# Optimization experiments

Measured on AMD Instinct MI355X. Metric: run time of the kernel, lower is better.

## Reference

```python
import math
import jax, jax.numpy as jnp
import numpy as np

NUM_HEADS = 16
D_MODEL = 1024
D_HEAD = 64
D_SEQ = 2048
NUM_LAYERS = 24
BATCH = 2


def setup_inputs() -> dict:
    key = jax.random.key(0)
    ks = jax.random.split(key, 10)
    s = math.sqrt(0.02)
    residual = jax.random.normal(ks[0], (BATCH, D_SEQ, D_MODEL), dtype=jnp.float32)
    W_Q = jax.random.normal(ks[1], (NUM_HEADS, D_MODEL, D_HEAD), dtype=jnp.float32) * s
    W_K = jax.random.normal(ks[2], (NUM_HEADS, D_MODEL, D_HEAD), dtype=jnp.float32) * s
    W_V = jax.random.normal(ks[3], (NUM_HEADS, D_MODEL, D_HEAD), dtype=jnp.float32) * s
    W_O = jax.random.normal(ks[4], (NUM_HEADS * D_HEAD, D_MODEL), dtype=jnp.float32) * s
    W_O = W_O / math.sqrt(NUM_LAYERS)
    b_Q = jax.random.normal(ks[5], (NUM_HEADS, D_HEAD), dtype=jnp.float32) * s
    b_K = jax.random.normal(ks[6], (NUM_HEADS, D_HEAD), dtype=jnp.float32) * s
    b_V = jax.random.normal(ks[7], (NUM_HEADS, D_HEAD), dtype=jnp.float32) * s
    b_O = jax.random.normal(ks[8], (D_MODEL,), dtype=jnp.float32) * s
    return dict(residual=residual, W_Q=W_Q, W_K=W_K, W_V=W_V, W_O=W_O,
                b_Q=b_Q, b_K=b_K, b_V=b_V, b_O=b_O)


def reference(residual, W_Q, W_K, W_V, W_O, b_Q, b_K, b_V, b_O):
    # residual: [b, s, m]; W_{Q,K,V}: [h, m, d]; b_{Q,K,V}: [h, d]
    Q = jnp.einsum('hmd,bsm->bshd', W_Q, residual) + b_Q
    K = jnp.einsum('hmd,bsm->bshd', W_K, residual) + b_K
    V = jnp.einsum('hmd,bsm->bshd', W_V, residual) + b_V
    # full causal score matrix [b, h, s_q, s_k], masked with -inf above diagonal
    QK = jnp.einsum('bqhd,bkhd->bhqk', Q, K)
    seq = residual.shape[1]
    causal = jnp.triu(jnp.ones((seq, seq), dtype=bool), k=1)  # True above diag
    QK_masked = jnp.where(causal, -jnp.inf, QK)
    soft = jax.nn.softmax(QK_masked / math.sqrt(D_HEAD), axis=-1)
    attn = jnp.einsum('bhqk,bkhd->bqhd', soft, V)  # [b, s, h, d]
    multi_head = attn.reshape(attn.shape[0], attn.shape[1], NUM_HEADS * D_HEAD)
    return jnp.einsum('em,bqe->bqm', W_O, multi_head) + b_O
```

## Files before the change

kernel.cpp:

```cpp
#include <hip/hip_runtime.h>
#include <stdint.h>

typedef unsigned short u16;
typedef _Float16 f16;
typedef __attribute__((ext_vector_type(8))) _Float16 f16x8;
typedef __attribute__((ext_vector_type(4))) float f32x4;
typedef __attribute__((ext_vector_type(4))) unsigned short u16x4;
typedef __attribute__((ext_vector_type(8))) unsigned short u16x8;
typedef __attribute__((ext_vector_type(2))) unsigned u32x2;

#define NHEADS 16
#define DMODEL 1024
#define DHEAD 64
#define SEQ 2048
#define NBATCH 2
#define MROWS (NBATCH * SEQ)
#define NQKV 3072
#define SCQ 0.18033688011112042f

__device__ __forceinline__ u16 f2h(float x) {
  union { f16 h; u16 u; } v;
  v.h = (f16)x;
  return v.u;
}

__device__ __forceinline__ void gload_lds16(const void* g, void* l) {
  __builtin_amdgcn_global_load_lds(
      (const __attribute__((address_space(1))) void*)g,
      (__attribute__((address_space(3))) void*)l, 16, 0, 0);
}

__global__ __launch_bounds__(256) void prep_kernel(
    const float* __restrict__ X,
    const float* __restrict__ WQ, const float* __restrict__ WK,
    const float* __restrict__ WV, const float* __restrict__ WO,
    u16* __restrict__ Xh, u16* __restrict__ Wqkv, u16* __restrict__ Wo) {
  __shared__ u16 lt[64][72];
  int blk = blockIdx.x;
  if (blk < 2048) {
    int i = blk * 256 + threadIdx.x;
    const f32x4* xv = (const f32x4*)(X + (size_t)i * 8);
    f32x4 a = xv[0], b = xv[1];
    u16x8 o;
    o[0] = f2h(a[0]); o[1] = f2h(a[1]); o[2] = f2h(a[2]); o[3] = f2h(a[3]);
    o[4] = f2h(b[0]); o[5] = f2h(b[1]); o[6] = f2h(b[2]); o[7] = f2h(b[3]);
    *(u16x8*)(Xh + (size_t)i * 8) = o;
  } else if (blk < 2816) {
    int bb = blk - 2048;
    int mt = bb & 15, hh = (bb >> 4) & 15, qkv = bb >> 8;
    const float* W = (qkv == 0) ? WQ : (qkv == 1) ? WK : WV;
    int m_in = threadIdx.x >> 2, dq = threadIdx.x & 3;
    const f32x4* sp4 = (const f32x4*)(W + (size_t)hh * (DMODEL * DHEAD) +
                                      (size_t)(mt * 64 + m_in) * DHEAD + dq * 16);
#pragma unroll
    for (int v4 = 0; v4 < 4; ++v4) {
      f32x4 a = sp4[v4];
#pragma unroll
      for (int j = 0; j < 4; ++j) lt[dq * 16 + v4 * 4 + j][m_in] = f2h(a[j]);
    }
    __syncthreads();
    int d_in = threadIdx.x >> 2, mq = threadIdx.x & 3;
    size_t orow = ((size_t)(qkv * 1024 + hh * 64 + d_in)) * DMODEL + mt * 64 + mq * 16;
    u16x8 o0, o1;
#pragma unroll
    for (int j = 0; j < 8; ++j) {
      o0[j] = lt[d_in][mq * 16 + j];
      o1[j] = lt[d_in][mq * 16 + 8 + j];
    }
    *(u16x8*)(Wqkv + orow) = o0;
    *(u16x8*)(Wqkv + orow + 8) = o1;
  } else {
    int bb = blk - 2816;
    int mt = bb & 15, et = bb >> 4;
    int e_in = threadIdx.x >> 2, mq = threadIdx.x & 3;
    const f32x4* sp4 = (const f32x4*)(WO + (size_t)(et * 64 + e_in) * DMODEL + mt * 64 + mq * 16);
#pragma unroll
    for (int v4 = 0; v4 < 4; ++v4) {
      f32x4 a = sp4[v4];
#pragma unroll
      for (int j = 0; j < 4; ++j) lt[mq * 16 + v4 * 4 + j][e_in] = f2h(a[j]);
    }
    __syncthreads();
    int m_in = threadIdx.x >> 2, eq = threadIdx.x & 3;
    size_t orow = (size_t)(mt * 64 + m_in) * DMODEL + et * 64 + eq * 16;
    u16x8 o0, o1;
#pragma unroll
    for (int j = 0; j < 8; ++j) {
      o0[j] = lt[m_in][eq * 16 + j];
      o1[j] = lt[m_in][eq * 16 + 8 + j];
    }
    *(u16x8*)(Wo + orow) = o0;
    *(u16x8*)(Wo + orow + 8) = o1;
  }
}

__global__ __launch_bounds__(256, 2) void gemm_qkv(
    const u16* __restrict__ A, const u16* __restrict__ Bt,
    const float* __restrict__ bq, const float* __restrict__ bk, const float* __restrict__ bv,
    u16* __restrict__ Qo, u16* __restrict__ Ko, u16* __restrict__ Vto) {
  __shared__ u16 lds[2][8192];
  const int tid = threadIdx.x;
  const int wid = tid >> 6, lane = tid & 63, lr = lane & 15, lg = lane >> 4;
  const int wr = wid >> 1, wc = wid & 1;
  const int brow = blockIdx.y * 128, bcol = blockIdx.x * 128;

  f32x4 acc[4][4];
#pragma unroll
  for (int i = 0; i < 4; ++i)
#pragma unroll
    for (int j = 0; j < 4; ++j) acc[i][j] = (f32x4){0.f, 0.f, 0.f, 0.f};

#define STAGE(buf, kt)                                                               \
  {                                                                                  \
    _Pragma("unroll") for (int i = 0; i < 2; ++i) {                                  \
      int idx = tid + i * 256;                                                       \
      gload_lds16(A + (size_t)(brow + (idx >> 2)) * 1024 + (kt) * 32 + (idx & 3) * 8,\
                  (char*)&lds[buf][0] + (wid * 64 + i * 256) * 16);                  \
    }                                                                                \
    _Pragma("unroll") for (int i = 0; i < 2; ++i) {                                  \
      int idx = tid + i * 256;                                                       \
      gload_lds16(Bt + (size_t)(bcol + (idx >> 2)) * 1024 + (kt) * 32 + (idx & 3) * 8,\
                  (char*)&lds[buf][4096] + (wid * 64 + i * 256) * 16);               \
    }                                                                                \
  }

  STAGE(0, 0);
  __syncthreads();
  int cur = 0;
  for (int kt = 0; kt < 32; ++kt) {
    if (kt + 1 < 32) STAGE(cur ^ 1, kt + 1);
    const u16* Ab = &lds[cur][0];
    const u16* Bb = &lds[cur][4096];
    f16x8 a[4], b[4];
#pragma unroll
    for (int ar = 0; ar < 4; ++ar)
      a[ar] = *(const f16x8*)(Ab + (wr * 64 + ar * 16 + lr) * 32 + lg * 8);
#pragma unroll
    for (int bc = 0; bc < 4; ++bc)
      b[bc] = *(const f16x8*)(Bb + (wc * 64 + bc * 16 + lr) * 32 + lg * 8);
#pragma unroll
    for (int ar = 0; ar < 4; ++ar)
#pragma unroll
      for (int bc = 0; bc < 4; ++bc)
        acc[ar][bc] = __builtin_amdgcn_mfma_f32_16x16x32_f16(a[ar], b[bc], acc[ar][bc], 0, 0, 0);
    __syncthreads();
    cur ^= 1;
  }

#pragma unroll
  for (int ar = 0; ar < 4; ++ar) {
    int row0 = brow + wr * 64 + ar * 16 + lg * 4;
    int bb = row0 >> 11, s0 = row0 & 2047;
#pragma unroll
    for (int bc = 0; bc < 4; ++bc) {
      int n = bcol + wc * 64 + bc * 16 + lr;
      int qkv = n >> 10, hd = n & 1023, h = hd >> 6, d = hd & 63;
      float bias = ((qkv == 0) ? bq : (qkv == 1) ? bk : bv)[hd];
      if (qkv < 2) {
        u16* dst = qkv ? Ko : Qo;
        float sc = qkv ? 1.f : SCQ;
        size_t base = ((size_t)(bb * NHEADS + h) * SEQ + s0) * DHEAD + d;
#pragma unroll
        for (int r = 0; r < 4; ++r)
          dst[base + (size_t)r * DHEAD] = f2h((acc[ar][bc][r] + bias) * sc);
      } else {
        u16x4 o;
        o[0] = f2h(acc[ar][bc][0] + bias);
        o[1] = f2h(acc[ar][bc][1] + bias);
        o[2] = f2h(acc[ar][bc][2] + bias);
        o[3] = f2h(acc[ar][bc][3] + bias);
        *(u16x4*)(Vto + ((size_t)(bb * NHEADS + h) * DHEAD + d) * SEQ + s0) = o;
      }
    }
  }
}

__global__ __launch_bounds__(256, 2) void gemm_out(
    const u16* __restrict__ A, const u16* __restrict__ Bt,
    const float* __restrict__ bo, float* __restrict__ Co) {
  __shared__ u16 lds[2][8192];
  const int tid = threadIdx.x;
  const int wid = tid >> 6, lane = tid & 63, lr = lane & 15, lg = lane >> 4;
  const int wr = wid >> 1, wc = wid & 1;
  const int brow = blockIdx.y * 128, bcol = blockIdx.x * 128;

  f32x4 acc[4][4];
#pragma unroll
  for (int i = 0; i < 4; ++i)
#pragma unroll
    for (int j = 0; j < 4; ++j) acc[i][j] = (f32x4){0.f, 0.f, 0.f, 0.f};

  STAGE(0, 0);
  __syncthreads();
  int cur = 0;
  for (int kt = 0; kt < 32; ++kt) {
    if (kt + 1 < 32) STAGE(cur ^ 1, kt + 1);
    const u16* Ab = &lds[cur][0];
    const u16* Bb = &lds[cur][4096];
    f16x8 a[4], b[4];
#pragma unroll
    for (int ar = 0; ar < 4; ++ar)
      a[ar] = *(const f16x8*)(Ab + (wr * 64 + ar * 16 + lr) * 32 + lg * 8);
#pragma unroll
    for (int bc = 0; bc < 4; ++bc)
      b[bc] = *(const f16x8*)(Bb + (wc * 64 + bc * 16 + lr) * 32 + lg * 8);
#pragma unroll
    for (int ar = 0; ar < 4; ++ar)
#pragma unroll
      for (int bc = 0; bc < 4; ++bc)
        acc[ar][bc] = __builtin_amdgcn_mfma_f32_16x16x32_f16(a[ar], b[bc], acc[ar][bc], 0, 0, 0);
    __syncthreads();
    cur ^= 1;
  }
#undef STAGE

#pragma unroll
  for (int ar = 0; ar < 4; ++ar) {
    int row0 = brow + wr * 64 + ar * 16 + lg * 4;
#pragma unroll
    for (int bc = 0; bc < 4; ++bc) {
      int n = bcol + wc * 64 + bc * 16 + lr;
      float bias = bo[n];
#pragma unroll
      for (int r = 0; r < 4; ++r)
        Co[(size_t)(row0 + r) * DMODEL + n] = acc[ar][bc][r] + bias;
    }
  }
}

__global__ __launch_bounds__(512, 4) void attn_kernel(
    const u16* __restrict__ Q, const u16* __restrict__ K,
    const u16* __restrict__ Vt, u16* __restrict__ MH) {
  __shared__ u16 sh[24576];
  char* sh8 = (char*)sh;
  const int tid = threadIdx.x, wid = tid >> 6, lane = tid & 63;
  const int lr = lane & 15, lg = lane >> 4;
  const int g = wid >> 2, ww = wid & 3;
  const int bid = blockIdx.x;
  const int x = bid & 7, y = bid >> 3;
  const int bh = x + 8 * (y & 3);
  const int p = y >> 2;
  const int h = bh & 15, b = bh >> 4;
  const int tA = 31 - p, tB = p;
  const int tg = g ? tB : tA;
  const u16* Qb = Q + (size_t)bh * (SEQ * DHEAD);
  const u16* Kb = K + (size_t)bh * (SEQ * DHEAD);
  const u16* Vb = Vt + (size_t)bh * (DHEAD * SEQ);

  const int srow = tid >> 3, sseg = (tid & 7) ^ (srow & 7);

#define KSTAGE(bufbyte, kt)                                              \
  gload_lds16(Kb + (size_t)((kt) * 64 + srow) * DHEAD + sseg * 8,        \
              sh8 + (bufbyte) + tid * 16);
#define VSTAGE(bufbyte, kt)                                              \
  gload_lds16(Vb + (size_t)srow * SEQ + (kt) * 64 + sseg * 8,            \
              sh8 + (bufbyte) + tid * 16);

  {
    gload_lds16(Qb + (size_t)(tA * 64 + srow) * DHEAD + sseg * 8, sh8 + 8192 + tid * 16);
    gload_lds16(Qb + (size_t)(tB * 64 + srow) * DHEAD + sseg * 8, sh8 + 24576 + tid * 16);
    KSTAGE(0, 0);
    VSTAGE(16384, 0);
  }
  __syncthreads();

  f16x8 qf[2];
  {
    const int base = g ? 24576 : 8192;
    const int row = ww * 16 + lr;
#pragma unroll
    for (int ks = 0; ks < 2; ++ks) {
      int off = (row * 128 + (ks * 4 + lg) * 16) ^ ((row & 7) << 4);
      qf[ks] = *(const f16x8*)(sh8 + base + off);
    }
  }
  __syncthreads();

  f32x4 acc_o[4];
#pragma unroll
  for (int z = 0; z < 4; ++z) acc_o[z] = (f32x4){0.f, 0.f, 0.f, 0.f};
  float m = -1e30f, l = 0.f;
  const int qlane = tg * 64 + ww * 16 + lr;
  char* pbase = sh8 + 32768 + wid * 2048;

  for (int kt = 0; kt <= tA; ++kt) {
    const int cur = kt & 1;
    if (kt + 1 <= tA) {
      KSTAGE((kt + 1) & 1 ? 8192 : 0, kt + 1);
      VSTAGE(((kt + 1) & 1) ? 24576 : 16384, kt + 1);
    }
    const bool act = (kt <= tg);
    const bool dg = (kt == tg);

    if (act) {
      const char* kb = sh8 + (cur ? 8192 : 0);
      f32x4 s4[4];
#pragma unroll
      for (int cb = 0; cb < 4; ++cb) s4[cb] = (f32x4){0.f, 0.f, 0.f, 0.f};
      __builtin_amdgcn_s_setprio(1);
#pragma unroll
      for (int ks = 0; ks < 2; ++ks)
#pragma unroll
        for (int cb = 0; cb < 4; ++cb) {
          int row = cb * 16 + lr;
          int off = (row * 128 + (ks * 4 + lg) * 16) ^ ((row & 7) << 4);
          f16x8 kf = *(const f16x8*)(kb + off);
          s4[cb] = __builtin_amdgcn_mfma_f32_16x16x32_f16(kf, qf[ks], s4[cb], 0, 0, 0);
        }
      __builtin_amdgcn_s_setprio(0);

      float tv[4][4];
#pragma unroll
      for (int cb = 0; cb < 4; ++cb)
#pragma unroll
        for (int r = 0; r < 4; ++r) {
          float v = s4[cb][r];
          if (dg && (kt * 64 + cb * 16 + lg * 4 + r > qlane)) v = -1e30f;
          tv[cb][r] = v;
        }
      float tm = tv[0][0];
#pragma unroll
      for (int cb = 0; cb < 4; ++cb)
#pragma unroll
        for (int r = 0; r < 4; ++r) tm = fmaxf(tm, tv[cb][r]);
      tm = fmaxf(tm, __shfl_xor(tm, 16));
      tm = fmaxf(tm, __shfl_xor(tm, 32));

      if (__all(tm <= m + 8.f)) {
        float rs = 0.f, pp[4][4];
#pragma unroll
        for (int cb = 0; cb < 4; ++cb)
#pragma unroll
          for (int r = 0; r < 4; ++r) {
            float pv = exp2f(tv[cb][r] - m);
            pp[cb][r] = pv;
            rs += pv;
          }
        rs += __shfl_xor(rs, 16);
        rs += __shfl_xor(rs, 32);
        l += rs;
#pragma unroll
        for (int cb = 0; cb < 4; ++cb) {
          u32x2 w;
          w[0] = (unsigned)f2h(pp[cb][0]) | ((unsigned)f2h(pp[cb][1]) << 16);
          w[1] = (unsigned)f2h(pp[cb][2]) | ((unsigned)f2h(pp[cb][3]) << 16);
          *(u32x2*)(pbase + ((lr * 128 + cb * 32 + lg * 8) ^ ((lr & 7) << 4))) = w;
        }
      } else {
        float m2 = fmaxf(m, tm);
        float al = exp2f(m - m2);
        m = m2;
        float rs = 0.f, pp[4][4];
#pragma unroll
        for (int cb = 0; cb < 4; ++cb)
#pragma unroll
          for (int r = 0; r < 4; ++r) {
            float pv = exp2f(tv[cb][r] - m2);
            pp[cb][r] = pv;
            rs += pv;
          }
        rs += __shfl_xor(rs, 16);
        rs += __shfl_xor(rs, 32);
        l = l * al + rs;
#pragma unroll
        for (int rr = 0; rr < 4; ++rr) {
          float ar = __shfl(al, (lg << 2) | rr);
#pragma unroll
          for (int db = 0; db < 4; ++db) acc_o[db][rr] *= ar;
        }
#pragma unroll
        for (int cb = 0; cb < 4; ++cb) {
          u32x2 w;
          w[0] = (unsigned)f2h(pp[cb][0]) | ((unsigned)f2h(pp[cb][1]) << 16);
          w[1] = (unsigned)f2h(pp[cb][2]) | ((unsigned)f2h(pp[cb][3]) << 16);
          *(u32x2*)(pbase + ((lr * 128 + cb * 32 + lg * 8) ^ ((lr & 7) << 4))) = w;
        }
      }

      const char* vbase = sh8 + (cur ? 24576 : 16384);
      __builtin_amdgcn_s_setprio(1);
#pragma unroll
      for (int ks = 0; ks < 2; ++ks) {
        f16x8 pa = *(const f16x8*)(pbase + ((lr * 128 + lg * 16 + ks * 64) ^ ((lr & 7) << 4)));
#pragma unroll
        for (int db = 0; db < 4; ++db) {
          int vrow = db * 16 + lr;
          f16x8 vv = *(const f16x8*)(vbase + ((vrow * 128 + lg * 16 + ks * 64) ^ ((vrow & 7) << 4)));
          acc_o[db] = __builtin_amdgcn_mfma_f32_16x16x32_f16(pa, vv, acc_o[db], 0, 0, 0);
        }
      }
      __builtin_amdgcn_s_setprio(0);

      if (dg) {
        float lb[4];
#pragma unroll
        for (int rr = 0; rr < 4; ++rr) lb[rr] = __shfl(l, (lg << 2) | rr);
#pragma unroll
        for (int db = 0; db < 4; ++db)
#pragma unroll
          for (int rr = 0; rr < 4; ++rr) {
            int qrow = tg * 64 + ww * 16 + lg * 4 + rr;
            MH[((size_t)(b * SEQ + qrow)) * DMODEL + h * DHEAD + db * 16 + lr] =
                f2h(acc_o[db][rr] / lb[rr]);
          }
      }
    }

    __syncthreads();
  }
#undef KSTAGE
#undef VSTAGE
}

extern "C" void kernel_launch(void* const* d_in, const int* in_sizes, int n_in,
                              void* d_out, int out_size, void* d_ws, size_t ws_size,
                              hipStream_t stream) {
  const float* residual = (const float*)d_in[0];
  const float* WQ = (const float*)d_in[1];
  const float* WK = (const float*)d_in[2];
  const float* WV = (const float*)d_in[3];
  const float* WO = (const float*)d_in[4];
  const float* bQ = (const float*)d_in[5];
  const float* bK = (const float*)d_in[6];
  const float* bV = (const float*)d_in[7];
  const float* bO = (const float*)d_in[8];
  float* out = (float*)d_out;

  char* w = (char*)d_ws;
  u16* Xh   = (u16*)(w);
  u16* Wqkv = (u16*)(w + ((size_t)8 << 20));
  u16* Wo   = (u16*)(w + ((size_t)14 << 20));
  u16* Qd   = (u16*)(w + ((size_t)16 << 20));
  u16* Kd   = (u16*)(w + ((size_t)24 << 20));
  u16* Vtd  = (u16*)(w + ((size_t)32 << 20));
  u16* MH   = (u16*)(w + ((size_t)40 << 20));

  prep_kernel<<<3072, 256, 0, stream>>>(residual, WQ, WK, WV, WO, Xh, Wqkv, Wo);

  gemm_qkv<<<dim3(NQKV / 128, MROWS / 128), 256, 0, stream>>>(
      Xh, Wqkv, bQ, bK, bV, Qd, Kd, Vtd);

  attn_kernel<<<512, 512, 0, stream>>>(Qd, Kd, Vtd, MH);

  gemm_out<<<dim3(DMODEL / 128, MROWS / 128), 256, 0, stream>>>(MH, Wo, bO, out);
}
```

Baseline: 119.7 us.

## Rewrite attention with 32x32 MFMA, register-resident P, one query tile per block

The attention kernel now uses 32x32x16 MFMA tiles, with each of two waves owning 32 query rows. The softmax probabilities are packed to fp16 in registers and fed straight into the PV MFMA, so the LDS round trip for P goes away. The launch changes from 512 blocks of 512 threads, each pairing a long and a short query tile, to 1024 blocks of 128 threads with one tile each, relying on the scheduler to balance the causal workload. The LDS swizzle pattern also changes, and dropping the tile pairing risks load imbalance and less K/V reuse per load.

```diff
diff --git a/kernel.cpp b/kernel.cpp
--- a/kernel.cpp
+++ b/kernel.cpp
@@ -2,12 +2,13 @@
 #include <stdint.h>
 
 typedef unsigned short u16;
+typedef unsigned long long u64;
 typedef _Float16 f16;
 typedef __attribute__((ext_vector_type(8))) _Float16 f16x8;
 typedef __attribute__((ext_vector_type(4))) float f32x4;
+typedef __attribute__((ext_vector_type(16))) float f32x16;
 typedef __attribute__((ext_vector_type(4))) unsigned short u16x4;
 typedef __attribute__((ext_vector_type(8))) unsigned short u16x8;
-typedef __attribute__((ext_vector_type(2))) unsigned u32x2;
 
 #define NHEADS 16
 #define DMODEL 1024
@@ -22,6 +23,26 @@
   union { f16 h; u16 u; } v;
   v.h = (f16)x;
   return v.u;
+}
+
+__device__ __forceinline__ unsigned pk2u(float x, float y) {
+  typedef __fp16 fp16x2 __attribute__((ext_vector_type(2)));
+  fp16x2 h = __builtin_amdgcn_cvt_pkrtz(x, y);
+  union { fp16x2 h; unsigned u; } v; v.h = h;
+  return v.u;
+}
+
+__device__ __forceinline__ f16x8 mkfrag(unsigned w0, unsigned w1, unsigned w2, unsigned w3) {
+  union { unsigned u[4]; f16x8 f; } t;
+  t.u[0] = w0; t.u[1] = w1; t.u[2] = w2; t.u[3] = w3;
+  return t.f;
+}
+
+__device__ __forceinline__ f16x8 vfrag(const char* row, int sz, int F, int hib8) {
+  union { u64 u[2]; f16x8 f; } t;
+  t.u[0] = *(const u64*)(row + (((2 * F) ^ sz) << 4) + hib8);
+  t.u[1] = *(const u64*)(row + (((2 * F + 1) ^ sz) << 4) + hib8);
+  return t.f;
 }
 
 __device__ __forceinline__ void gload_lds16(const void* g, void* l) {
@@ -228,188 +249,165 @@
   }
 }
 
-__global__ __launch_bounds__(512, 4) void attn_kernel(
+__global__ __launch_bounds__(128, 2) void attn_kernel(
     const u16* __restrict__ Q, const u16* __restrict__ K,
     const u16* __restrict__ Vt, u16* __restrict__ MH) {
-  __shared__ u16 sh[24576];
-  char* sh8 = (char*)sh;
+  __shared__ char sh8[32768];
   const int tid = threadIdx.x, wid = tid >> 6, lane = tid & 63;
-  const int lr = lane & 15, lg = lane >> 4;
-  const int g = wid >> 2, ww = wid & 3;
+  const int l31 = lane & 31, hi = lane >> 5;
   const int bid = blockIdx.x;
-  const int x = bid & 7, y = bid >> 3;
-  const int bh = x + 8 * (y & 3);
-  const int p = y >> 2;
+  const int x = bid & 7, r = bid >> 3;
+  const int bh = x + 8 * (r & 3);
+  const int t = 31 - (r >> 2);
   const int h = bh & 15, b = bh >> 4;
-  const int tA = 31 - p, tB = p;
-  const int tg = g ? tB : tA;
   const u16* Qb = Q + (size_t)bh * (SEQ * DHEAD);
   const u16* Kb = K + (size_t)bh * (SEQ * DHEAD);
   const u16* Vb = Vt + (size_t)bh * (DHEAD * SEQ);
 
-  const int srow = tid >> 3, sseg = (tid & 7) ^ (srow & 7);
-
-#define KSTAGE(bufbyte, kt)                                              \
-  gload_lds16(Kb + (size_t)((kt) * 64 + srow) * DHEAD + sseg * 8,        \
-              sh8 + (bufbyte) + tid * 16);
-#define VSTAGE(bufbyte, kt)                                              \
-  gload_lds16(Vb + (size_t)srow * SEQ + (kt) * 64 + sseg * 8,            \
-              sh8 + (bufbyte) + tid * 16);
-
+#pragma unroll
+  for (int i = 0; i < 4; ++i) {
+    int idx = tid + i * 128, row = idx >> 3;
+    int sseg = (idx & 7) ^ ((row ^ (row >> 3)) & 7);
+    gload_lds16(Qb + (size_t)(t * 64 + row) * DHEAD + sseg * 8, sh8 + 8192 + idx * 16);
+    gload_lds16(Kb + (size_t)row * DHEAD + sseg * 8, sh8 + idx * 16);
+    gload_lds16(Vb + (size_t)row * SEQ + sseg * 8, sh8 + 16384 + idx * 16);
+  }
+  __syncthreads();
+
+  f16x8 qf0, qf1, qf2, qf3;
   {
-    gload_lds16(Qb + (size_t)(tA * 64 + srow) * DHEAD + sseg * 8, sh8 + 8192 + tid * 16);
-    gload_lds16(Qb + (size_t)(tB * 64 + srow) * DHEAD + sseg * 8, sh8 + 24576 + tid * 16);
-    KSTAGE(0, 0);
-    VSTAGE(16384, 0);
+    int row = (wid << 5) + l31;
+    int swz = ((row ^ (row >> 3)) & 7) << 4;
+    const char* qb = sh8 + 8192 + row * 128;
+    qf0 = *(const f16x8*)(qb + ((hi * 16 + 0)  ^ swz));
+    qf1 = *(const f16x8*)(qb + ((hi * 16 + 32) ^ swz));
+    qf2 = *(const f16x8*)(qb + ((hi * 16 + 64) ^ swz));
+    qf3 = *(const f16x8*)(qb + ((hi * 16 + 96) ^ swz));
   }
   __syncthreads();
 
-  f16x8 qf[2];
-  {
-    const int base = g ? 24576 : 8192;
-    const int row = ww * 16 + lr;
-#pragma unroll
-    for (int ks = 0; ks < 2; ++ks) {
-      int off = (row * 128 + (ks * 4 + lg) * 16) ^ ((row & 7) << 4);
-      qf[ks] = *(const f16x8*)(sh8 + base + off);
-    }
-  }
-  __syncthreads();
-
-  f32x4 acc_o[4];
-#pragma unroll
-  for (int z = 0; z < 4; ++z) acc_o[z] = (f32x4){0.f, 0.f, 0.f, 0.f};
+  f32x16 acc0, acc1;
+#pragma unroll
+  for (int z = 0; z < 16; ++z) { acc0[z] = 0.f; acc1[z] = 0.f; }
   float m = -1e30f, l = 0.f;
-  const int qlane = tg * 64 + ww * 16 + lr;
-  char* pbase = sh8 + 32768 + wid * 2048;
-
-  for (int kt = 0; kt <= tA; ++kt) {
-    const int cur = kt & 1;
-    if (kt + 1 <= tA) {
-      KSTAGE((kt + 1) & 1 ? 8192 : 0, kt + 1);
-      VSTAGE(((kt + 1) & 1) ? 24576 : 16384, kt + 1);
-    }
-    const bool act = (kt <= tg);
-    const bool dg = (kt == tg);
-
-    if (act) {
-      const char* kb = sh8 + (cur ? 8192 : 0);
-      f32x4 s4[4];
-#pragma unroll
-      for (int cb = 0; cb < 4; ++cb) s4[cb] = (f32x4){0.f, 0.f, 0.f, 0.f};
+  const int qa = t * 64 + (wid << 5) + l31;
+
+  const int sw0 = (l31 ^ (l31 >> 3)) & 7;
+  const int kz0 = sw0 << 4;
+  const int r32 = 32 + l31;
+  const int sw1 = (r32 ^ (r32 >> 3)) & 7;
+  const int kz1 = sw1 << 4;
+  const int hib = hi * 16;
+  const int hib8 = hi * 8;
+
+  for (int kt = 0; kt <= t; ++kt) {
+    if (kt < t) {
+      const int kb_n = ((kt + 1) & 1) ? 8192 : 0;
+      const int vb_n = ((kt + 1) & 1) ? 24576 : 16384;
+#pragma unroll
+      for (int i = 0; i < 4; ++i) {
+        int idx = tid + i * 128, rw = idx >> 3;
+        int sseg = (idx & 7) ^ ((rw ^ (rw >> 3)) & 7);
+        gload_lds16(Kb + (size_t)((kt + 1) * 64 + rw) * DHEAD + sseg * 8, sh8 + kb_n + idx * 16);
+        gload_lds16(Vb + (size_t)rw * SEQ + (kt + 1) * 64 + sseg * 8, sh8 + vb_n + idx * 16);
+      }
+    }
+    const char* kbuf = sh8 + ((kt & 1) ? 8192 : 0);
+    const char* vbuf = sh8 + ((kt & 1) ? 24576 : 16384);
+
+    f32x16 s0, s1;
+#pragma unroll
+    for (int z = 0; z < 16; ++z) { s0[z] = 0.f; s1[z] = 0.f; }
+    {
+      const char* kb0 = kbuf + l31 * 128;
+      const char* kb1 = kbuf + r32 * 128;
+      f16x8 kf;
       __builtin_amdgcn_s_setprio(1);
-#pragma unroll
-      for (int ks = 0; ks < 2; ++ks)
-#pragma unroll
-        for (int cb = 0; cb < 4; ++cb) {
-          int row = cb * 16 + lr;
-          int off = (row * 128 + (ks * 4 + lg) * 16) ^ ((row & 7) << 4);
-          f16x8 kf = *(const f16x8*)(kb + off);
-          s4[cb] = __builtin_amdgcn_mfma_f32_16x16x32_f16(kf, qf[ks], s4[cb], 0, 0, 0);
-        }
+      kf = *(const f16x8*)(kb0 + ((hib + 0)  ^ kz0)); s0 = __builtin_amdgcn_mfma_f32_32x32x16_f16(kf, qf0, s0, 0, 0, 0);
+      kf = *(const f16x8*)(kb0 + ((hib + 32) ^ kz0)); s0 = __builtin_amdgcn_mfma_f32_32x32x16_f16(kf, qf1, s0, 0, 0, 0);
+      kf = *(const f16x8*)(kb0 + ((hib + 64) ^ kz0)); s0 = __builtin_amdgcn_mfma_f32_32x32x16_f16(kf, qf2, s0, 0, 0, 0);
+      kf = *(const f16x8*)(kb0 + ((hib + 96) ^ kz0)); s0 = __builtin_amdgcn_mfma_f32_32x32x16_f16(kf, qf3, s0, 0, 0, 0);
+      kf = *(const f16x8*)(kb1 + ((hib + 0)  ^ kz1)); s1 = __builtin_amdgcn_mfma_f32_32x32x16_f16(kf, qf0, s1, 0, 0, 0);
+      kf = *(const f16x8*)(kb1 + ((hib + 32) ^ kz1)); s1 = __builtin_amdgcn_mfma_f32_32x32x16_f16(kf, qf1, s1, 0, 0, 0);
+      kf = *(const f16x8*)(kb1 + ((hib + 64) ^ kz1)); s1 = __builtin_amdgcn_mfma_f32_32x32x16_f16(kf, qf2, s1, 0, 0, 0);
+      kf = *(const f16x8*)(kb1 + ((hib + 96) ^ kz1)); s1 = __builtin_amdgcn_mfma_f32_32x32x16_f16(kf, qf3, s1, 0, 0, 0);
       __builtin_amdgcn_s_setprio(0);
-
-      float tv[4][4];
-#pragma unroll
-      for (int cb = 0; cb < 4; ++cb)
-#pragma unroll
-        for (int r = 0; r < 4; ++r) {
-          float v = s4[cb][r];
-          if (dg && (kt * 64 + cb * 16 + lg * 4 + r > qlane)) v = -1e30f;
-          tv[cb][r] = v;
-        }
-      float tm = tv[0][0];
-#pragma unroll
-      for (int cb = 0; cb < 4; ++cb)
-#pragma unroll
-        for (int r = 0; r < 4; ++r) tm = fmaxf(tm, tv[cb][r]);
-      tm = fmaxf(tm, __shfl_xor(tm, 16));
-      tm = fmaxf(tm, __shfl_xor(tm, 32));
-
-      if (__all(tm <= m + 8.f)) {
-        float rs = 0.f, pp[4][4];
-#pragma unroll
-        for (int cb = 0; cb < 4; ++cb)
-#pragma unroll
-          for (int r = 0; r < 4; ++r) {
-            float pv = exp2f(tv[cb][r] - m);
-            pp[cb][r] = pv;
-            rs += pv;
-          }
-        rs += __shfl_xor(rs, 16);
-        rs += __shfl_xor(rs, 32);
-        l += rs;
-#pragma unroll
-        for (int cb = 0; cb < 4; ++cb) {
-          u32x2 w;
-          w[0] = (unsigned)f2h(pp[cb][0]) | ((unsigned)f2h(pp[cb][1]) << 16);
-          w[1] = (unsigned)f2h(pp[cb][2]) | ((unsigned)f2h(pp[cb][3]) << 16);
-          *(u32x2*)(pbase + ((lr * 128 + cb * 32 + lg * 8) ^ ((lr & 7) << 4))) = w;
-        }
-      } else {
-        float m2 = fmaxf(m, tm);
-        float al = exp2f(m - m2);
-        m = m2;
-        float rs = 0.f, pp[4][4];
-#pragma unroll
-        for (int cb = 0; cb < 4; ++cb)
-#pragma unroll
-          for (int r = 0; r < 4; ++r) {
-            float pv = exp2f(tv[cb][r] - m2);
-            pp[cb][r] = pv;
-            rs += pv;
-          }
-        rs += __shfl_xor(rs, 16);
-        rs += __shfl_xor(rs, 32);
-        l = l * al + rs;
-#pragma unroll
-        for (int rr = 0; rr < 4; ++rr) {
-          float ar = __shfl(al, (lg << 2) | rr);
-#pragma unroll
-          for (int db = 0; db < 4; ++db) acc_o[db][rr] *= ar;
-        }
-#pragma unroll
-        for (int cb = 0; cb < 4; ++cb) {
-          u32x2 w;
-          w[0] = (unsigned)f2h(pp[cb][0]) | ((unsigned)f2h(pp[cb][1]) << 16);
-          w[1] = (unsigned)f2h(pp[cb][2]) | ((unsigned)f2h(pp[cb][3]) << 16);
-          *(u32x2*)(pbase + ((lr * 128 + cb * 32 + lg * 8) ^ ((lr & 7) << 4))) = w;
-        }
+    }
+
+    if (kt == t) {
+#pragma unroll
+      for (int rr = 0; rr < 16; ++rr) {
+        int k0 = kt * 64 + (rr & 3) + 8 * (rr >> 2) + 4 * hi;
+        if (k0 > qa) s0[rr] = -1e30f;
+        if (k0 + 32 > qa) s1[rr] = -1e30f;
       }
-
-      const char* vbase = sh8 + (cur ? 24576 : 16384);
+    }
+
+    float tm = s0[0];
+#pragma unroll
+    for (int rr = 1; rr < 16; ++rr) tm = fmaxf(tm, s0[rr]);
+#pragma unroll
+    for (int rr = 0; rr < 16; ++rr) tm = fmaxf(tm, s1[rr]);
+    tm = fmaxf(tm, __shfl_xor(tm, 32));
+
+    if (!__all(tm <= m + 8.f)) {
+      float m2 = fmaxf(m, tm);
+      float al = exp2f(m - m2);
+      m = m2;
+      l *= al;
+#pragma unroll
+      for (int rr = 0; rr < 16; ++rr) {
+        int qp = (rr & 3) + 8 * (rr >> 2) + 4 * hi;
+        float af = __shfl(al, qp);
+        acc0[rr] *= af;
+        acc1[rr] *= af;
+      }
+    }
+
+    float rs = 0.f;
+#pragma unroll
+    for (int rr = 0; rr < 16; ++rr) { s0[rr] = exp2f(s0[rr] - m); rs += s0[rr]; }
+#pragma unroll
+    for (int rr = 0; rr < 16; ++rr) { s1[rr] = exp2f(s1[rr] - m); rs += s1[rr]; }
+    rs += __shfl_xor(rs, 32);
+    l += rs;
+
+    f16x8 pa0 = mkfrag(pk2u(s0[0],  s0[1]),  pk2u(s0[2],  s0[3]),
+                       pk2u(s0[4],  s0[5]),  pk2u(s0[6],  s0[7]));
+    f16x8 pa1 = mkfrag(pk2u(s0[8],  s0[9]),  pk2u(s0[10], s0[11]),
+                       pk2u(s0[12], s0[13]), pk2u(s0[14], s0[15]));
+    f16x8 pa2 = mkfrag(pk2u(s1[0],  s1[1]),  pk2u(s1[2],  s1[3]),
+                       pk2u(s1[4],  s1[5]),  pk2u(s1[6],  s1[7]));
+    f16x8 pa3 = mkfrag(pk2u(s1[8],  s1[9]),  pk2u(s1[10], s1[11]),
+                       pk2u(s1[12], s1[13]), pk2u(s1[14], s1[15]));
+
+    {
+      const char* vr0 = vbuf + l31 * 128;
+      const char* vr1 = vbuf + r32 * 128;
       __builtin_amdgcn_s_setprio(1);
-#pragma unroll
-      for (int ks = 0; ks < 2; ++ks) {
-        f16x8 pa = *(const f16x8*)(pbase + ((lr * 128 + lg * 16 + ks * 64) ^ ((lr & 7) << 4)));
-#pragma unroll
-        for (int db = 0; db < 4; ++db) {
-          int vrow = db * 16 + lr;
-          f16x8 vv = *(const f16x8*)(vbase + ((vrow * 128 + lg * 16 + ks * 64) ^ ((vrow & 7) << 4)));
-          acc_o[db] = __builtin_amdgcn_mfma_f32_16x16x32_f16(pa, vv, acc_o[db], 0, 0, 0);
-        }
-      }
+      acc0 = __builtin_amdgcn_mfma_f32_32x32x16_f16(pa0, vfrag(vr0, sw0, 0, hib8), acc0, 0, 0, 0);
+      acc0 = __builtin_amdgcn_mfma_f32_32x32x16_f16(pa1, vfrag(vr0, sw0, 1, hib8), acc0, 0, 0, 0);
+      acc0 = __builtin_amdgcn_mfma_f32_32x32x16_f16(pa2, vfrag(vr0, sw0, 2, hib8), acc0, 0, 0, 0);
+      acc0 = __builtin_amdgcn_mfma_f32_32x32x16_f16(pa3, vfrag(vr0, sw0, 3, hib8), acc0, 0, 0, 0);
+      acc1 = __builtin_amdgcn_mfma_f32_32x32x16_f16(pa0, vfrag(vr1, sw1, 0, hib8), acc1, 0, 0, 0);
+      acc1 = __builtin_amdgcn_mfma_f32_32x32x16_f16(pa1, vfrag(vr1, sw1, 1, hib8), acc1, 0, 0, 0);
+      acc1 = __builtin_amdgcn_mfma_f32_32x32x16_f16(pa2, vfrag(vr1, sw1, 2, hib8), acc1, 0, 0, 0);
+      acc1 = __builtin_amdgcn_mfma_f32_32x32x16_f16(pa3, vfrag(vr1, sw1, 3, hib8), acc1, 0, 0, 0);
       __builtin_amdgcn_s_setprio(0);
-
-      if (dg) {
-        float lb[4];
-#pragma unroll
-        for (int rr = 0; rr < 4; ++rr) lb[rr] = __shfl(l, (lg << 2) | rr);
-#pragma unroll
-        for (int db = 0; db < 4; ++db)
-#pragma unroll
-          for (int rr = 0; rr < 4; ++rr) {
-            int qrow = tg * 64 + ww * 16 + lg * 4 + rr;
-            MH[((size_t)(b * SEQ + qrow)) * DMODEL + h * DHEAD + db * 16 + lr] =
-                f2h(acc_o[db][rr] / lb[rr]);
-          }
-      }
     }
 
     __syncthreads();
   }
-#undef KSTAGE
-#undef VSTAGE
+
+#pragma unroll
+  for (int rr = 0; rr < 16; ++rr) {
+    int qp = (rr & 3) + 8 * (rr >> 2) + 4 * hi;
+    float ls = __shfl(l, qp);
+    int qrow = t * 64 + (wid << 5) + qp;
+    size_t base = ((size_t)(b * SEQ) + qrow) * DMODEL + h * DHEAD;
+    MH[base + l31]      = f2h(acc0[rr] / ls);
+    MH[base + 32 + l31] = f2h(acc1[rr] / ls);
+  }
 }
 
 extern "C" void kernel_launch(void* const* d_in, const int* in_sizes, int n_in,
@@ -440,7 +438,7 @@
   gemm_qkv<<<dim3(NQKV / 128, MROWS / 128), 256, 0, stream>>>(
       Xh, Wqkv, bQ, bK, bV, Qd, Kd, Vtd);
 
-  attn_kernel<<<512, 512, 0, stream>>>(Qd, Kd, Vtd, MH);
+  attn_kernel<<<1024, 128, 0, stream>>>(Qd, Kd, Vtd, MH);
 
   gemm_out<<<dim3(DMODEL / 128, MROWS / 128), 256, 0, stream>>>(MH, Wo, bO, out);
 }
```

Result: slower. 129.9 us (+8.5%).
